# Optimization experiments

Measured on AMD Instinct MI355X. Metric: run time of the kernel, lower is better.

## Reference

```python
import math
import jax, jax.numpy as jnp
import numpy as np

B, L, D, H = 4, 2048, 1024, 16
DH = D // H  # head dim = 64
PAD_LEN = 128  # trailing padded positions


def setup_inputs() -> dict:
    key = jax.random.key(0)
    ks = jax.random.split(key, 12)
    q = jax.random.normal(ks[0], (B, L, D), dtype=jnp.float32)
    k = jax.random.normal(ks[1], (B, L, D), dtype=jnp.float32)
    v = jax.random.normal(ks[2], (B, L, D), dtype=jnp.float32)
    # additive causal mask: 0 on/below diagonal, -inf above
    causal = jnp.triu(jnp.ones((L, L), dtype=bool), k=1)
    att_mask = jnp.where(causal, -jnp.inf, 0.0).astype(jnp.float32)
    # boolean pad mask over key positions: last PAD_LEN positions are padding
    pad_mask = (jnp.arange(L) >= (L - PAD_LEN))[None, :].repeat(B, axis=0)
    s = 0.02
    params = {
        'w_q': jax.random.normal(ks[3], (D, D), jnp.float32) * s,
        'b_q': jnp.zeros((D,), jnp.float32),
        'w_k': jax.random.normal(ks[4], (D, D), jnp.float32) * s,
        'b_k': jnp.zeros((D,), jnp.float32),
        'w_v': jax.random.normal(ks[5], (D, D), jnp.float32) * s,
        'b_v': jnp.zeros((D,), jnp.float32),
        'w_out': jax.random.normal(ks[6], (D, D), jnp.float32) * s,
        'b_out': jnp.zeros((D,), jnp.float32),
    }
    return {'q': q, 'k': k, 'v': v, 'att_mask': att_mask, 'pad_mask': pad_mask, **params}


def reference(q, k, v, att_mask, pad_mask, w_q, b_q, w_k, b_k, w_v, b_v, w_out, b_out):
    b, l, d = q.shape
    qp = q @ w_q.T + b_q
    kp = k @ w_k.T + b_k  # computed but unused below: source stacks q for k and v (faithful)
    vp = v @ w_v.T + b_v  # computed but unused below (faithful to source bug)
    # split(ndim//nhead, dim=2) + stack(dim=1) == reshape + transpose -> [B,H,L,DH]
    qh = qp.reshape(b, l, H, DH).transpose(0, 2, 1, 3)
    kh = qh  # source: torch.stack(q, ...) used for k
    vh = qh  # source: torch.stack(q, ...) used for v
    att = jnp.einsum('bhqd,bhkd->bhqk', qh, kh) / math.sqrt(DH)
    att = att + att_mask  # broadcast [L,L] over [B,H,L,L]
    # pad_mask [B,L] over keys, broadcast across heads and query positions
    att = jnp.where(pad_mask[:, None, None, :], -jnp.inf, att)
    p = jax.nn.softmax(att, axis=-1)
    o = jnp.einsum('bhqk,bhkd->bhqd', p, vh)
    o = o.transpose(0, 2, 1, 3).reshape(b, l, d)
    return o @ w_out.T + b_out
```

## Files before the change

kernel.cpp:

```cpp
#include <hip/hip_runtime.h>
#include <math.h>


typedef __attribute__((ext_vector_type(8))) short bf16x8;
typedef __attribute__((ext_vector_type(8))) unsigned short u16x8;
typedef __attribute__((ext_vector_type(4))) float f32x4;
typedef __attribute__((ext_vector_type(2))) unsigned int u32x2;

#define MFMA16(a, b, c) __builtin_amdgcn_mfma_f32_16x16x32_bf16(a, b, c, 0, 0, 0)

#define GLDS16(g, l) __builtin_amdgcn_global_load_lds(                        \
    (const __attribute__((address_space(1))) unsigned int*)(g),               \
    (__attribute__((address_space(3))) unsigned int*)(l), 16, 0, 0)

__device__ __forceinline__ unsigned short f2bf(float f) {
    union { float f; unsigned int u; } x; x.f = f;
    unsigned int u = x.u + 0x7fffu + ((x.u >> 16) & 1u);
    return (unsigned short)(u >> 16);
}

__device__ __forceinline__ unsigned int pack_bf16(float lo, float hi) {
    union { float f; unsigned int u; } a, b;
    a.f = lo; b.f = hi;
    return __builtin_amdgcn_perm(b.u + 0x8000u, a.u + 0x8000u, 0x07060302u);
}

__global__ __launch_bounds__(256) void cast3_bf16(
    const float* __restrict__ s0, unsigned short* __restrict__ d0,
    const float* __restrict__ s1, unsigned short* __restrict__ d1,
    const float* __restrict__ s2, unsigned short* __restrict__ d2)
{
    const float* s; unsigned short* d; int i;
    int blk = blockIdx.x;
    if (blk < 4096)      { s = s0; d = d0; i = (blk * 256 + threadIdx.x) * 8; }
    else if (blk < 4608) { s = s1; d = d1; i = ((blk - 4096) * 256 + threadIdx.x) * 8; }
    else                 { s = s2; d = d2; i = ((blk - 4608) * 256 + threadIdx.x) * 8; }
    f32x4 a = *(const f32x4*)(s + i);
    f32x4 b = *(const f32x4*)(s + i + 4);
    u16x8 o;
    o[0] = f2bf(a[0]); o[1] = f2bf(a[1]); o[2] = f2bf(a[2]); o[3] = f2bf(a[3]);
    o[4] = f2bf(b[0]); o[5] = f2bf(b[1]); o[6] = f2bf(b[2]); o[7] = f2bf(b[3]);
    *(u16x8*)(d + i) = o;
}

__global__ __launch_bounds__(256) void gemm_bt(
    const unsigned short* __restrict__ A,
    const unsigned short* __restrict__ Bw,
    const float* __restrict__ bias,
    unsigned short* __restrict__ Cbf,
    float* __restrict__ Cf,
    int M, int N, int K, int mode)
{
    __shared__ __align__(16) short lA[2][128 * 64];
    __shared__ __align__(16) short lB[2][128 * 64];
    const int tid = threadIdx.x;
    const int lane = tid & 63, w = tid >> 6;
    const int quad = lane >> 4, l16 = lane & 15;
    const int m0 = blockIdx.y * 128, n0 = blockIdx.x * 128;
    const int wm = (w >> 1) * 64, wn = (w & 1) * 64;

    const int r8 = lane >> 3;
    const int ch = (lane & 7) ^ r8;
    const unsigned short* Ag = A  + (size_t)(m0 + w * 32 + r8) * K + ch * 8;
    const unsigned short* Bg = Bw + (size_t)(n0 + w * 32 + r8) * K + ch * 8;

    f32x4 acc[4][4];
#pragma unroll
    for (int i = 0; i < 4; ++i)
#pragma unroll
        for (int j = 0; j < 4; ++j) acc[i][j] = (f32x4){0.f, 0.f, 0.f, 0.f};

    auto prefetch = [&](int k0, int buf) {
#pragma unroll
        for (int j = 0; j < 4; ++j) {
            GLDS16(Ag + (size_t)j * 8 * K + k0, &lA[buf][(w * 32 + j * 8) * 64]);
            GLDS16(Bg + (size_t)j * 8 * K + k0, &lB[buf][(w * 32 + j * 8) * 64]);
        }
    };
    auto compute = [&](int buf) {
#pragma unroll
        for (int ks = 0; ks < 2; ++ks) {
            const int kc = (ks << 2) + quad;
            const int sw = (kc ^ (l16 & 7)) * 8;
            bf16x8 af[4], bfr[4];
#pragma unroll
            for (int i = 0; i < 4; ++i)
                af[i] = *(bf16x8*)&lA[buf][(wm + i * 16 + l16) * 64 + sw];
#pragma unroll
            for (int j = 0; j < 4; ++j)
                bfr[j] = *(bf16x8*)&lB[buf][(wn + j * 16 + l16) * 64 + sw];
#pragma unroll
            for (int i = 0; i < 4; ++i)
#pragma unroll
                for (int j = 0; j < 4; ++j)
                    acc[i][j] = MFMA16(af[i], bfr[j], acc[i][j]);
        }
    };

    const int niter = K >> 6;
    prefetch(0, 0);
    for (int k = 0; k < niter; k += 2) {
        __syncthreads();
        if (k + 1 < niter) prefetch((k + 1) << 6, 1);
        compute(0);
        __syncthreads();
        if (k + 2 < niter) prefetch((k + 2) << 6, 0);
        if (k + 1 < niter) compute(1);
    }

#pragma unroll
    for (int i = 0; i < 4; ++i)
#pragma unroll
        for (int j = 0; j < 4; ++j) {
            int col = n0 + wn + j * 16 + l16;
            float bv = bias[col];
#pragma unroll
            for (int r = 0; r < 4; ++r) {
                int row = m0 + wm + i * 16 + quad * 4 + r;
                float v = acc[i][j][r] + bv;
                if (mode == 0) {
                    int b = row >> 11, l = row & 2047;
                    int h = col >> 6, dh = col & 63;
                    Cbf[(((size_t)(b * 16 + h) * 2048) + l) * 64 + dh] = f2bf(v);
                } else {
                    Cf[(size_t)row * N + col] = v;
                }
            }
        }
}

__global__ __launch_bounds__(256, 4) void attn_kernel(
    const unsigned short* __restrict__ qh,
    unsigned short* __restrict__ obf)
{
    __shared__ __align__(16) short kv [64 * 72];
    __shared__ __align__(16) short kvT[64 * 72];
    __shared__ __align__(16) short pls[128 * 72];
    const int tid = threadIdx.x;
    const int lane = tid & 63, w = tid >> 6;
    const int quad = lane >> 4, l16 = lane & 15;
    const int bh = blockIdx.x & 63;
    const int g = blockIdx.x >> 6;
    const int ga = g >> 2, gb = g & 3;
    const int qt2 = (ga == 0) ? 15 - gb : (ga == 1) ? 8 + gb : (ga == 2) ? 7 - gb : gb;
    const int rbase = qt2 << 7;
    const unsigned short* __restrict__ base = qh + ((size_t)bh << 17);

    bf16x8 bq[2][2];
    int rmin[2];
#pragma unroll
    for (int s = 0; s < 2; ++s) {
        rmin[s] = rbase + w * 32 + s * 16;
        const unsigned short* qrow = base + (size_t)(rmin[s] + l16) * 64 + quad * 8;
        bq[s][0] = *(const bf16x8*)qrow;
        bq[s][1] = *(const bf16x8*)(qrow + 32);
    }

    float lsum[2] = {0.f, 0.f};
    f32x4 oacc[2][4];
#pragma unroll
    for (int s = 0; s < 2; ++s)
#pragma unroll
        for (int t = 0; t < 4; ++t) oacc[s][t] = (f32x4){0.f, 0.f, 0.f, 0.f};

    const int nkt = min(2 * qt2 + 2, 30);
    const float c = 0.18033688011f;
    short* pw0 = pls + (w * 2 + 0) * (16 * 72);
    short* pw1 = pls + (w * 2 + 1) * (16 * 72);

    for (int kt = 0; kt < nkt; ++kt) {
        const int kb = kt << 6;
        __syncthreads();
        const unsigned short* src = base + (size_t)(kb + lane) * 64 + w * 16;
        u16x8 d0 = *(const u16x8*)src;
        u16x8 d1 = *(const u16x8*)(src + 8);
        *(u16x8*)&kv[lane * 72 + w * 16]     = d0;
        *(u16x8*)&kv[lane * 72 + w * 16 + 8] = d1;
#pragma unroll
        for (int j = 0; j < 8; ++j) kvT[(w * 16 + j) * 72 + lane]     = d0[j];
#pragma unroll
        for (int j = 0; j < 8; ++j) kvT[(w * 16 + 8 + j) * 72 + lane] = d1[j];
        __syncthreads();

        const bool act0 = (kb <= rmin[0] + 15);
        const bool act1 = (kb <= rmin[1] + 15);
        const bool dg0 = (kb + 63 > rmin[0]);
        const bool dg1 = (kb + 63 > rmin[1]);

#pragma unroll
        for (int t = 0; t < 4; ++t) {
            bf16x8 fk0 = *(bf16x8*)&kv[(t * 16 + l16) * 72 + quad * 8];
            bf16x8 fk1 = *(bf16x8*)&kv[(t * 16 + l16) * 72 + 32 + quad * 8];
            const int keyb = kb + t * 16 + 4 * quad;
#pragma unroll
            for (int s = 0; s < 2; ++s) {
                if (!(s ? act1 : act0)) continue;
                f32x4 sv = (f32x4){0.f, 0.f, 0.f, 0.f};
                sv = MFMA16(fk0, bq[s][0], sv);
                sv = MFMA16(fk1, bq[s][1], sv);
                const bool dgs = s ? dg1 : dg0;
                const int qg = rmin[s] + l16;
                float p[4];
#pragma unroll
                for (int r = 0; r < 4; ++r) {
                    float pv = exp2f(sv[r] * c);
                    if (dgs && (keyb + r > qg)) pv = 0.f;
                    p[r] = pv;
                    lsum[s] += pv;
                }
                u32x2 pk;
                pk[0] = pack_bf16(p[0], p[1]);
                pk[1] = pack_bf16(p[2], p[3]);
                short* pws = s ? pw1 : pw0;
                *(u32x2*)&pws[l16 * 72 + t * 16 + 4 * quad] = pk;
            }
        }

#pragma unroll
        for (int ks = 0; ks < 2; ++ks) {
            bf16x8 bp0, bp1;
            if (act0) bp0 = *(bf16x8*)&pw0[l16 * 72 + ks * 32 + quad * 8];
            if (act1) bp1 = *(bf16x8*)&pw1[l16 * 72 + ks * 32 + quad * 8];
#pragma unroll
            for (int t2 = 0; t2 < 4; ++t2) {
                bf16x8 av = *(bf16x8*)&kvT[(t2 * 16 + l16) * 72 + ks * 32 + quad * 8];
                if (act0) oacc[0][t2] = MFMA16(av, bp0, oacc[0][t2]);
                if (act1) oacc[1][t2] = MFMA16(av, bp1, oacc[1][t2]);
            }
        }
    }

    const int b = bh >> 4, h = bh & 15;
#pragma unroll
    for (int s = 0; s < 2; ++s) {
        float rs = lsum[s];
        rs += __shfl_xor(rs, 16);
        rs += __shfl_xor(rs, 32);
        const float inv = 1.f / rs;
        unsigned short* orow = obf + ((size_t)(b * 2048 + rmin[s] + l16)) * 1024
                             + h * 64 + 4 * quad;
#pragma unroll
        for (int t2 = 0; t2 < 4; ++t2) {
            u32x2 pk;
            pk[0] = pack_bf16(oacc[s][t2][0] * inv, oacc[s][t2][1] * inv);
            pk[1] = pack_bf16(oacc[s][t2][2] * inv, oacc[s][t2][3] * inv);
            *(u32x2*)(orow + t2 * 16) = pk;
        }
    }
}

extern "C" void kernel_launch(void* const* d_in, const int* in_sizes, int n_in,
                              void* d_out, int out_size, void* d_ws, size_t ws_size,
                              hipStream_t stream) {
    const float* q     = (const float*)d_in[0];
    const float* w_q   = (const float*)d_in[5];
    const float* b_q   = (const float*)d_in[6];
    const float* w_out = (const float*)d_in[11];
    const float* b_out = (const float*)d_in[12];
    float* out = (float*)d_out;

    char* ws = (char*)d_ws;
    unsigned short* a_bf   = (unsigned short*)ws;
    unsigned short* wq_bf  = (unsigned short*)(ws + (16u << 20));
    unsigned short* wo_bf  = (unsigned short*)(ws + (18u << 20));
    unsigned short* qheads = (unsigned short*)(ws + (20u << 20));
    unsigned short* o_bf   = a_bf;

    hipLaunchKernelGGL(cast3_bf16, dim3(5120), dim3(256), 0, stream,
                       q, a_bf, w_q, wq_bf, w_out, wo_bf);

    hipLaunchKernelGGL(gemm_bt, dim3(8, 64), dim3(256), 0, stream,
                       a_bf, wq_bf, b_q, qheads, (float*)nullptr, 8192, 1024, 1024, 0);
    hipLaunchKernelGGL(attn_kernel, dim3(1024), dim3(256), 0, stream, qheads, o_bf);
    hipLaunchKernelGGL(gemm_bt, dim3(8, 64), dim3(256), 0, stream,
                       o_bf, wo_bf, b_out, (unsigned short*)nullptr, out, 8192, 1024, 1024, 1);
}
```

Before: 285.1 us.

## Fold softmax scale into Q projection, MFMA row sums, prefetch K tile, swizzle GEMM grid

The Q projection epilogue now pre-scales Q by sqrt(c) so the attention scores feed exp2 directly without a per-element multiply. The output is rescaled by the inverse factor, and row sums come from an MFMA against a ones vector instead of scalar adds and shuffles. The next K/V tile is loaded into registers during compute, the barrier is split into an explicit waitcnt plus s_barrier with setprio, bf16 packing uses the hardware v_cvt_pk_bf16_f32 instruction, and GEMM blocks are remapped for locality. Rounding changes slightly because the scale is applied before the bf16 cast of Q.

```diff
diff --git a/kernel.cpp b/kernel.cpp
--- a/kernel.cpp
+++ b/kernel.cpp
@@ -13,16 +13,19 @@
     (const __attribute__((address_space(1))) unsigned int*)(g),               \
     (__attribute__((address_space(3))) unsigned int*)(l), 16, 0, 0)
 
+#define SCALE_Q   0.42466092f
+#define INV_SCALE 2.3548202f
+
 __device__ __forceinline__ unsigned short f2bf(float f) {
     union { float f; unsigned int u; } x; x.f = f;
     unsigned int u = x.u + 0x7fffu + ((x.u >> 16) & 1u);
     return (unsigned short)(u >> 16);
 }
 
-__device__ __forceinline__ unsigned int pack_bf16(float lo, float hi) {
-    union { float f; unsigned int u; } a, b;
-    a.f = lo; b.f = hi;
-    return __builtin_amdgcn_perm(b.u + 0x8000u, a.u + 0x8000u, 0x07060302u);
+__device__ __forceinline__ unsigned int cvt_pk_bf16(float lo, float hi) {
+    unsigned int r;
+    asm("v_cvt_pk_bf16_f32 %0, %1, %2" : "=v"(r) : "v"(lo), "v"(hi));
+    return r;
 }
 
 __global__ __launch_bounds__(256) void cast3_bf16(
@@ -56,7 +59,9 @@
     const int tid = threadIdx.x;
     const int lane = tid & 63, w = tid >> 6;
     const int quad = lane >> 4, l16 = lane & 15;
-    const int m0 = blockIdx.y * 128, n0 = blockIdx.x * 128;
+    const int flat = blockIdx.y * 8 + blockIdx.x;
+    const int lf = (flat & 7) * 64 + (flat >> 3);
+    const int m0 = (lf >> 3) * 128, n0 = (lf & 7) * 128;
     const int wm = (w >> 1) * 64, wn = (w & 1) * 64;
 
     const int r8 = lane >> 3;
@@ -121,7 +126,7 @@
                 if (mode == 0) {
                     int b = row >> 11, l = row & 2047;
                     int h = col >> 6, dh = col & 63;
-                    Cbf[(((size_t)(b * 16 + h) * 2048) + l) * 64 + dh] = f2bf(v);
+                    Cbf[(((size_t)(b * 16 + h) * 2048) + l) * 64 + dh] = f2bf(v * SCALE_Q);
                 } else {
                     Cf[(size_t)row * N + col] = v;
                 }
@@ -156,31 +161,51 @@
         bq[s][1] = *(const bf16x8*)(qrow + 32);
     }
 
-    float lsum[2] = {0.f, 0.f};
     f32x4 oacc[2][4];
-#pragma unroll
-    for (int s = 0; s < 2; ++s)
+    f32x4 sacc[2];
+#pragma unroll
+    for (int s = 0; s < 2; ++s) {
+        sacc[s] = (f32x4){0.f, 0.f, 0.f, 0.f};
 #pragma unroll
         for (int t = 0; t < 4; ++t) oacc[s][t] = (f32x4){0.f, 0.f, 0.f, 0.f};
+    }
+
+    bf16x8 ones;
+#pragma unroll
+    for (int j = 0; j < 8; ++j) ones[j] = (short)0x3F80;
 
     const int nkt = min(2 * qt2 + 2, 30);
-    const float c = 0.18033688011f;
     short* pw0 = pls + (w * 2 + 0) * (16 * 72);
     short* pw1 = pls + (w * 2 + 1) * (16 * 72);
+
+    u16x8 d0, d1;
+    {
+        const unsigned short* src = base + (size_t)lane * 64 + w * 16;
+        d0 = *(const u16x8*)src;
+        d1 = *(const u16x8*)(src + 8);
+    }
 
     for (int kt = 0; kt < nkt; ++kt) {
         const int kb = kt << 6;
         __syncthreads();
-        const unsigned short* src = base + (size_t)(kb + lane) * 64 + w * 16;
-        u16x8 d0 = *(const u16x8*)src;
-        u16x8 d1 = *(const u16x8*)(src + 8);
         *(u16x8*)&kv[lane * 72 + w * 16]     = d0;
         *(u16x8*)&kv[lane * 72 + w * 16 + 8] = d1;
 #pragma unroll
         for (int j = 0; j < 8; ++j) kvT[(w * 16 + j) * 72 + lane]     = d0[j];
 #pragma unroll
         for (int j = 0; j < 8; ++j) kvT[(w * 16 + 8 + j) * 72 + lane] = d1[j];
-        __syncthreads();
+        asm volatile("s_waitcnt lgkmcnt(0)" ::: "memory");
+        __builtin_amdgcn_s_barrier();
+        asm volatile("" ::: "memory");
+        __builtin_amdgcn_sched_barrier(0);
+
+        if (kt + 1 < nkt) {
+            const unsigned short* src = base + (size_t)(kb + 64 + lane) * 64 + w * 16;
+            d0 = *(const u16x8*)src;
+            d1 = *(const u16x8*)(src + 8);
+        }
+
+        __builtin_amdgcn_s_setprio(1);
 
         const bool act0 = (kb <= rmin[0] + 15);
         const bool act1 = (kb <= rmin[1] + 15);
@@ -203,14 +228,13 @@
                 float p[4];
 #pragma unroll
                 for (int r = 0; r < 4; ++r) {
-                    float pv = exp2f(sv[r] * c);
+                    float pv = exp2f(sv[r]);
                     if (dgs && (keyb + r > qg)) pv = 0.f;
                     p[r] = pv;
-                    lsum[s] += pv;
                 }
                 u32x2 pk;
-                pk[0] = pack_bf16(p[0], p[1]);
-                pk[1] = pack_bf16(p[2], p[3]);
+                pk[0] = cvt_pk_bf16(p[0], p[1]);
+                pk[1] = cvt_pk_bf16(p[2], p[3]);
                 short* pws = s ? pw1 : pw0;
                 *(u32x2*)&pws[l16 * 72 + t * 16 + 4 * quad] = pk;
             }
@@ -221,6 +245,8 @@
             bf16x8 bp0, bp1;
             if (act0) bp0 = *(bf16x8*)&pw0[l16 * 72 + ks * 32 + quad * 8];
             if (act1) bp1 = *(bf16x8*)&pw1[l16 * 72 + ks * 32 + quad * 8];
+            if (act0) sacc[0] = MFMA16(ones, bp0, sacc[0]);
+            if (act1) sacc[1] = MFMA16(ones, bp1, sacc[1]);
 #pragma unroll
             for (int t2 = 0; t2 < 4; ++t2) {
                 bf16x8 av = *(bf16x8*)&kvT[(t2 * 16 + l16) * 72 + ks * 32 + quad * 8];
@@ -228,22 +254,20 @@
                 if (act1) oacc[1][t2] = MFMA16(av, bp1, oacc[1][t2]);
             }
         }
+        __builtin_amdgcn_s_setprio(0);
     }
 
     const int b = bh >> 4, h = bh & 15;
 #pragma unroll
     for (int s = 0; s < 2; ++s) {
-        float rs = lsum[s];
-        rs += __shfl_xor(rs, 16);
-        rs += __shfl_xor(rs, 32);
-        const float inv = 1.f / rs;
+        const float inv = INV_SCALE / sacc[s][0];
         unsigned short* orow = obf + ((size_t)(b * 2048 + rmin[s] + l16)) * 1024
                              + h * 64 + 4 * quad;
 #pragma unroll
         for (int t2 = 0; t2 < 4; ++t2) {
             u32x2 pk;
-            pk[0] = pack_bf16(oacc[s][t2][0] * inv, oacc[s][t2][1] * inv);
-            pk[1] = pack_bf16(oacc[s][t2][2] * inv, oacc[s][t2][3] * inv);
+            pk[0] = cvt_pk_bf16(oacc[s][t2][0] * inv, oacc[s][t2][1] * inv);
+            pk[1] = cvt_pk_bf16(oacc[s][t2][2] * inv, oacc[s][t2][3] * inv);
             *(u32x2*)(orow + t2 * 16) = pk;
         }
     }
```

New measurement: 272.0 us. 1.05x faster.
